# Optimization experiments

Hardware: AMD Instinct MI355X
Metric: run time of the kernel (lower is better)

Reference implementation:

```python
import jax, jax.numpy as jnp
import numpy as np

B = 1_000_000  # number of tracklets
STATE_DIM, OBS_DIM = 6, 3


def setup_inputs() -> dict:
    key = jax.random.key(0)
    k1, k2, k3, k4 = jax.random.split(key, 4)
    x = jax.random.normal(k1, (B, STATE_DIM, 1), dtype=jnp.float32)
    # P: symmetric PSD covariance, eye + small random A A^T
    A = 0.1 * jax.random.normal(k2, (B, STATE_DIM, STATE_DIM), dtype=jnp.float32)
    P = jnp.einsum('bij,bkj->bik', A, A) + jnp.eye(STATE_DIM, dtype=jnp.float32)
    delta_t = jax.random.uniform(k3, (B,), dtype=jnp.float32, minval=0.01, maxval=0.2)
    Q = jnp.broadcast_to(0.01 * jnp.eye(STATE_DIM, dtype=jnp.float32), (B, STATE_DIM, STATE_DIM))
    z = jax.random.normal(k4, (B, OBS_DIM, 1), dtype=jnp.float32)
    R = jnp.broadcast_to(0.1 * jnp.eye(OBS_DIM, dtype=jnp.float32), (B, OBS_DIM, OBS_DIM))
    return {"x": x, "P": P, "delta_t": delta_t, "Q": Q, "z": z, "R": R}


def reference(x, P, delta_t, Q, z, R):
    """One batched EKF step: predict(delta_t, Q) then update(z, R).
    Returns (x_upd [B,6,1], P_upd [B,6,6])."""
    Bn = x.shape[0]
    dt = delta_t.reshape(-1)
    # F = I6 with dt on the (pos, vel) off-diagonal entries (0,3),(1,4),(2,5)
    shift = jnp.zeros((STATE_DIM, STATE_DIM), x.dtype).at[
        jnp.array([0, 1, 2]), jnp.array([3, 4, 5])].set(1.0)
    F = jnp.eye(STATE_DIM, dtype=x.dtype) + dt[:, None, None] * shift  # [B,6,6]

    # Predict
    x_pred = F @ x                                           # [B,6,1]
    P_pred = F @ P @ jnp.swapaxes(F, -1, -2) + Q             # [B,6,6]

    # Update (H selects first 3 state rows, so H@P == P[:, :3, :], etc.)
    S = P_pred[:, :OBS_DIM, :OBS_DIM] + R                    # [B,3,3]
    K = P_pred[:, :, :OBS_DIM] @ jnp.linalg.inv(S)           # [B,6,3]
    innov = z - x_pred[:, :OBS_DIM, :]                       # [B,3,1]
    x_upd = x_pred + K @ innov                               # [B,6,1]
    # K @ H places K in the first 3 columns of a [B,6,6] matrix
    KH = jnp.concatenate([K, jnp.zeros((Bn, STATE_DIM, STATE_DIM - OBS_DIM), x.dtype)], axis=2)
    P_upd = P_pred - KH @ P_pred                             # (I - K H) P
    return x_upd, P_upd
```

## Files before the change

kernel.cpp:

```cpp
#include <hip/hip_runtime.h>


__global__ __launch_bounds__(256)
void ekf_step_kernel(const float* __restrict__ x_in,
                     const float* __restrict__ P_in,
                     const float* __restrict__ dt_in,
                     const float* __restrict__ Q_in,
                     const float* __restrict__ z_in,
                     const float* __restrict__ R_in,
                     float* __restrict__ x_out,
                     float* __restrict__ P_out,
                     int B)
{
    const int t = blockIdx.x * blockDim.x + threadIdx.x;
    if (t >= B) return;

    const float dt = dt_in[t];

    float x[6];
    {
        const float2* p = (const float2*)(x_in + (size_t)t * 6);
        float2 a = p[0], b = p[1], c = p[2];
        x[0] = a.x; x[1] = a.y; x[2] = b.x; x[3] = b.y; x[4] = c.x; x[5] = c.y;
    }
    float z[3];
    {
        const float* p = z_in + (size_t)t * 3;
        z[0] = p[0]; z[1] = p[1]; z[2] = p[2];
    }
    float P[36];
    {
        const float4* p = (const float4*)(P_in + (size_t)t * 36);
#pragma unroll
        for (int k = 0; k < 9; ++k) {
            float4 v = p[k];
            P[4*k+0] = v.x; P[4*k+1] = v.y; P[4*k+2] = v.z; P[4*k+3] = v.w;
        }
    }

    float xp[6];
#pragma unroll
    for (int i = 0; i < 3; ++i) xp[i] = fmaf(dt, x[i+3], x[i]);
    xp[3] = x[3]; xp[4] = x[4]; xp[5] = x[5];

    float FP[36];
#pragma unroll
    for (int i = 0; i < 6; ++i) {
#pragma unroll
        for (int j = 0; j < 6; ++j) {
            float v = P[i*6 + j];
            if (i < 3) v = fmaf(dt, P[(i+3)*6 + j], v);
            FP[i*6 + j] = v;
        }
    }

    float Q[36];
    {
        const float4* p = (const float4*)(Q_in + (size_t)t * 36);
#pragma unroll
        for (int k = 0; k < 9; ++k) {
            float4 v = p[k];
            Q[4*k+0] = v.x; Q[4*k+1] = v.y; Q[4*k+2] = v.z; Q[4*k+3] = v.w;
        }
    }
    float Pp[36];
#pragma unroll
    for (int i = 0; i < 6; ++i) {
#pragma unroll
        for (int j = 0; j < 6; ++j) {
            float v = FP[i*6 + j];
            if (j < 3) v = fmaf(dt, FP[i*6 + j + 3], v);
            Pp[i*6 + j] = v + Q[i*6 + j];
        }
    }

    float R[9];
    {
        const float* p = R_in + (size_t)t * 9;
#pragma unroll
        for (int k = 0; k < 9; ++k) R[k] = p[k];
    }

    const float S00 = Pp[0]  + R[0], S01 = Pp[1]  + R[1], S02 = Pp[2]  + R[2];
    const float S10 = Pp[6]  + R[3], S11 = Pp[7]  + R[4], S12 = Pp[8]  + R[5];
    const float S20 = Pp[12] + R[6], S21 = Pp[13] + R[7], S22 = Pp[14] + R[8];

    const float c00 =  (S11*S22 - S12*S21);
    const float c01 = -(S10*S22 - S12*S20);
    const float c02 =  (S10*S21 - S11*S20);
    const float c10 = -(S01*S22 - S02*S21);
    const float c11 =  (S00*S22 - S02*S20);
    const float c12 = -(S00*S21 - S01*S20);
    const float c20 =  (S01*S12 - S02*S11);
    const float c21 = -(S00*S12 - S02*S10);
    const float c22 =  (S00*S11 - S01*S10);
    const float det  = S00*c00 + S01*c01 + S02*c02;
    const float rdet = 1.0f / det;

    float Si[9];
    Si[0] = c00*rdet; Si[1] = c10*rdet; Si[2] = c20*rdet;
    Si[3] = c01*rdet; Si[4] = c11*rdet; Si[5] = c21*rdet;
    Si[6] = c02*rdet; Si[7] = c12*rdet; Si[8] = c22*rdet;

    float K[18];
#pragma unroll
    for (int i = 0; i < 6; ++i) {
#pragma unroll
        for (int a = 0; a < 3; ++a) {
            K[i*3 + a] = Pp[i*6 + 0] * Si[0*3 + a]
                       + Pp[i*6 + 1] * Si[1*3 + a]
                       + Pp[i*6 + 2] * Si[2*3 + a];
        }
    }

    const float iv0 = z[0] - xp[0];
    const float iv1 = z[1] - xp[1];
    const float iv2 = z[2] - xp[2];

    float xu[6];
#pragma unroll
    for (int i = 0; i < 6; ++i) {
        xu[i] = xp[i] + K[i*3+0]*iv0 + K[i*3+1]*iv1 + K[i*3+2]*iv2;
    }

    float Pu[36];
#pragma unroll
    for (int i = 0; i < 6; ++i) {
#pragma unroll
        for (int j = 0; j < 6; ++j) {
            Pu[i*6 + j] = Pp[i*6 + j]
                        - (K[i*3+0]*Pp[0*6 + j] + K[i*3+1]*Pp[6 + j] + K[i*3+2]*Pp[12 + j]);
        }
    }

    {
        float2* p = (float2*)(x_out + (size_t)t * 6);
        p[0] = make_float2(xu[0], xu[1]);
        p[1] = make_float2(xu[2], xu[3]);
        p[2] = make_float2(xu[4], xu[5]);
    }
    {
        float4* p = (float4*)(P_out + (size_t)t * 36);
#pragma unroll
        for (int k = 0; k < 9; ++k) {
            p[k] = make_float4(Pu[4*k+0], Pu[4*k+1], Pu[4*k+2], Pu[4*k+3]);
        }
    }
}

extern "C" void kernel_launch(void* const* d_in, const int* in_sizes, int n_in,
                              void* d_out, int out_size, void* d_ws, size_t ws_size,
                              hipStream_t stream) {
    const float* x_in  = (const float*)d_in[0];
    const float* P_in  = (const float*)d_in[1];
    const float* dt_in = (const float*)d_in[2];
    const float* Q_in  = (const float*)d_in[3];
    const float* z_in  = (const float*)d_in[4];
    const float* R_in  = (const float*)d_in[5];

    const int B = in_sizes[2];

    float* x_out = (float*)d_out;
    float* P_out = (float*)d_out + (size_t)B * 6;

    const int block = 256;
    const int grid = (B + block - 1) / block;
    ekf_step_kernel<<<grid, block, 0, stream>>>(x_in, P_in, dt_in, Q_in, z_in, R_in,
                                                x_out, P_out, B);
}
```

Measured before the change: 435.0 us.

## Stage P, Q, R loads and P stores through padded shared memory for coalescing

Replaces the strided per-thread float4 loads of P and Q, the scalar loads of R, and the strided float4 stores of P_out with block-cooperative coalesced accesses. Each block stages these arrays through a padded shared-memory tile (stride 37 or 11) to transpose between the row-per-thread layout and contiguous global order. The goal is fully coalesced global transactions on a bandwidth-bound kernel. In exchange it adds shared-memory traffic, several __syncthreads barriers, about 37 KB of LDS per block, and a launch-bounds occupancy hint.

```diff
diff --git a/kernel.cpp b/kernel.cpp
--- a/kernel.cpp
+++ b/kernel.cpp
@@ -1,7 +1,11 @@
 #include <hip/hip_runtime.h>
 
 
-__global__ __launch_bounds__(256)
+#define BLK  256
+#define PADP 37
+#define PADR 11
+
+__global__ __launch_bounds__(BLK, 4)
 void ekf_step_kernel(const float* __restrict__ x_in,
                      const float* __restrict__ P_in,
                      const float* __restrict__ dt_in,
@@ -12,36 +16,64 @@
                      float* __restrict__ P_out,
                      int B)
 {
-    const int t = blockIdx.x * blockDim.x + threadIdx.x;
-    if (t >= B) return;
-
-    const float dt = dt_in[t];
-
-    float x[6];
-    {
+    __shared__ float sm[BLK * PADP];
+
+    const int tid = threadIdx.x;
+    const int b0  = blockIdx.x * BLK;
+    const int t   = b0 + tid;
+    const bool valid = (t < B);
+    const int  nval  = min(BLK, B - b0);
+    const int  lim4  = nval * 9;
+
+    const float dt = valid ? dt_in[t] : 0.0f;
+
+    float x[6] = {0,0,0,0,0,0};
+    if (valid) {
         const float2* p = (const float2*)(x_in + (size_t)t * 6);
         float2 a = p[0], b = p[1], c = p[2];
-        x[0] = a.x; x[1] = a.y; x[2] = b.x; x[3] = b.y; x[4] = c.x; x[5] = c.y;
-    }
-    float z[3];
-    {
+        x[0]=a.x; x[1]=a.y; x[2]=b.x; x[3]=b.y; x[4]=c.x; x[5]=c.y;
+    }
+    float zv[3] = {0,0,0};
+    if (valid) {
         const float* p = z_in + (size_t)t * 3;
-        z[0] = p[0]; z[1] = p[1]; z[2] = p[2];
-    }
+        zv[0]=p[0]; zv[1]=p[1]; zv[2]=p[2];
+    }
+
+    {
+        const float4* gp = (const float4*)P_in + (size_t)b0 * 9;
+#pragma unroll
+        for (int k = 0; k < 9; ++k) {
+            int m = tid + k*BLK;
+            float4 v = make_float4(0.f,0.f,0.f,0.f);
+            if (m < lim4) v = gp[m];
+            int r = m / 9, c = m - r*9;
+            float* d = &sm[r*PADP + c*4];
+            d[0]=v.x; d[1]=v.y; d[2]=v.z; d[3]=v.w;
+        }
+    }
+    __syncthreads();
     float P[36];
-    {
-        const float4* p = (const float4*)(P_in + (size_t)t * 36);
-#pragma unroll
-        for (int k = 0; k < 9; ++k) {
-            float4 v = p[k];
-            P[4*k+0] = v.x; P[4*k+1] = v.y; P[4*k+2] = v.z; P[4*k+3] = v.w;
+#pragma unroll
+    for (int j = 0; j < 36; ++j) P[j] = sm[tid*PADP + j];
+    __syncthreads();
+
+    {
+        const float4* gq = (const float4*)Q_in + (size_t)b0 * 9;
+#pragma unroll
+        for (int k = 0; k < 9; ++k) {
+            int m = tid + k*BLK;
+            float4 v = make_float4(0.f,0.f,0.f,0.f);
+            if (m < lim4) v = gq[m];
+            int r = m / 9, c = m - r*9;
+            float* d = &sm[r*PADP + c*4];
+            d[0]=v.x; d[1]=v.y; d[2]=v.z; d[3]=v.w;
         }
     }
 
     float xp[6];
 #pragma unroll
     for (int i = 0; i < 3; ++i) xp[i] = fmaf(dt, x[i+3], x[i]);
-    xp[3] = x[3]; xp[4] = x[4]; xp[5] = x[5];
+    xp[3]=x[3]; xp[4]=x[4]; xp[5]=x[5];
 
     float FP[36];
 #pragma unroll
@@ -54,15 +86,8 @@
         }
     }
 
-    float Q[36];
-    {
-        const float4* p = (const float4*)(Q_in + (size_t)t * 36);
-#pragma unroll
-        for (int k = 0; k < 9; ++k) {
-            float4 v = p[k];
-            Q[4*k+0] = v.x; Q[4*k+1] = v.y; Q[4*k+2] = v.z; Q[4*k+3] = v.w;
-        }
-    }
+    __syncthreads();
+
     float Pp[36];
 #pragma unroll
     for (int i = 0; i < 6; ++i) {
@@ -70,16 +95,28 @@
         for (int j = 0; j < 6; ++j) {
             float v = FP[i*6 + j];
             if (j < 3) v = fmaf(dt, FP[i*6 + j + 3], v);
-            Pp[i*6 + j] = v + Q[i*6 + j];
-        }
-    }
-
+            Pp[i*6 + j] = v + sm[tid*PADP + i*6 + j];
+        }
+    }
+    __syncthreads();
+
+    {
+        const float* gr = R_in + (size_t)b0 * 9;
+        const int limf = nval * 9;
+#pragma unroll
+        for (int k = 0; k < 9; ++k) {
+            int m = tid + k*BLK;
+            float v = 0.f;
+            if (m < limf) v = gr[m];
+            int r = m / 9, c = m - r*9;
+            sm[r*PADR + c] = v;
+        }
+    }
+    __syncthreads();
     float R[9];
-    {
-        const float* p = R_in + (size_t)t * 9;
-#pragma unroll
-        for (int k = 0; k < 9; ++k) R[k] = p[k];
-    }
+#pragma unroll
+    for (int j = 0; j < 9; ++j) R[j] = sm[tid*PADR + j];
+    __syncthreads();
 
     const float S00 = Pp[0]  + R[0], S01 = Pp[1]  + R[1], S02 = Pp[2]  + R[2];
     const float S10 = Pp[6]  + R[3], S11 = Pp[7]  + R[4], S12 = Pp[8]  + R[5];
@@ -98,52 +135,56 @@
     const float rdet = 1.0f / det;
 
     float Si[9];
-    Si[0] = c00*rdet; Si[1] = c10*rdet; Si[2] = c20*rdet;
-    Si[3] = c01*rdet; Si[4] = c11*rdet; Si[5] = c21*rdet;
-    Si[6] = c02*rdet; Si[7] = c12*rdet; Si[8] = c22*rdet;
+    Si[0]=c00*rdet; Si[1]=c10*rdet; Si[2]=c20*rdet;
+    Si[3]=c01*rdet; Si[4]=c11*rdet; Si[5]=c21*rdet;
+    Si[6]=c02*rdet; Si[7]=c12*rdet; Si[8]=c22*rdet;
 
     float K[18];
 #pragma unroll
     for (int i = 0; i < 6; ++i) {
 #pragma unroll
         for (int a = 0; a < 3; ++a) {
-            K[i*3 + a] = Pp[i*6 + 0] * Si[0*3 + a]
-                       + Pp[i*6 + 1] * Si[1*3 + a]
-                       + Pp[i*6 + 2] * Si[2*3 + a];
-        }
-    }
-
-    const float iv0 = z[0] - xp[0];
-    const float iv1 = z[1] - xp[1];
-    const float iv2 = z[2] - xp[2];
+            K[i*3+a] = Pp[i*6+0]*Si[0*3+a] + Pp[i*6+1]*Si[1*3+a] + Pp[i*6+2]*Si[2*3+a];
+        }
+    }
+
+    const float iv0 = zv[0] - xp[0];
+    const float iv1 = zv[1] - xp[1];
+    const float iv2 = zv[2] - xp[2];
 
     float xu[6];
 #pragma unroll
-    for (int i = 0; i < 6; ++i) {
+    for (int i = 0; i < 6; ++i)
         xu[i] = xp[i] + K[i*3+0]*iv0 + K[i*3+1]*iv1 + K[i*3+2]*iv2;
-    }
-
-    float Pu[36];
+
 #pragma unroll
     for (int i = 0; i < 6; ++i) {
 #pragma unroll
         for (int j = 0; j < 6; ++j) {
-            Pu[i*6 + j] = Pp[i*6 + j]
-                        - (K[i*3+0]*Pp[0*6 + j] + K[i*3+1]*Pp[6 + j] + K[i*3+2]*Pp[12 + j]);
-        }
-    }
-
-    {
+            sm[tid*PADP + i*6 + j] =
+                Pp[i*6 + j] - (K[i*3+0]*Pp[j] + K[i*3+1]*Pp[6+j] + K[i*3+2]*Pp[12+j]);
+        }
+    }
+
+    if (valid) {
         float2* p = (float2*)(x_out + (size_t)t * 6);
         p[0] = make_float2(xu[0], xu[1]);
         p[1] = make_float2(xu[2], xu[3]);
         p[2] = make_float2(xu[4], xu[5]);
     }
-    {
-        float4* p = (float4*)(P_out + (size_t)t * 36);
-#pragma unroll
-        for (int k = 0; k < 9; ++k) {
-            p[k] = make_float4(Pu[4*k+0], Pu[4*k+1], Pu[4*k+2], Pu[4*k+3]);
+
+    __syncthreads();
+
+    {
+        float4* gp = (float4*)P_out + (size_t)b0 * 9;
+#pragma unroll
+        for (int k = 0; k < 9; ++k) {
+            int m = tid + k*BLK;
+            if (m < lim4) {
+                int r = m / 9, c = m - r*9;
+                const float* s = &sm[r*PADP + c*4];
+                gp[m] = make_float4(s[0], s[1], s[2], s[3]);
+            }
         }
     }
 }
@@ -163,8 +204,7 @@
     float* x_out = (float*)d_out;
     float* P_out = (float*)d_out + (size_t)B * 6;
 
-    const int block = 256;
-    const int grid = (B + block - 1) / block;
-    ekf_step_kernel<<<grid, block, 0, stream>>>(x_in, P_in, dt_in, Q_in, z_in, R_in,
-                                                x_out, P_out, B);
+    const int grid = (B + BLK - 1) / BLK;
+    ekf_step_kernel<<<grid, BLK, 0, stream>>>(x_in, P_in, dt_in, Q_in, z_in, R_in,
+                                              x_out, P_out, B);
 }
```

Result: faster. 417.7 us (-4.0%).
